# Performance work log

Measured on AMD Instinct MI355X. Metric: run time of the kernel, lower is better.

## Reference

```python
import jax, jax.numpy as jnp
import numpy as np

CLIP = 10.0  # tanh clipping constant (Kool et al. C=10)


def setup_inputs() -> dict:
    key = jax.random.key(0)
    kq, kk, kv, km = jax.random.split(key, 4)
    B, M, N, D = 16, 2048, 2048, 128
    Q = jax.random.normal(kq, (B, M, D), dtype=jnp.float32)
    K = jax.random.normal(kk, (B, N, D), dtype=jnp.float32)
    V = jax.random.normal(kv, (B, N, D), dtype=jnp.float32)
    # mask: [B, N, 1] bool; True means "forbidden" (set logit to -inf).
    # p=0.3 so every row keeps plenty of valid keys (no all-masked rows).
    mask = jax.random.bernoulli(km, 0.3, (B, N, 1))
    return {"Q": Q, "K": K, "V": V, "mask": mask}


def reference(Q, K, V, mask):
    d_k = jnp.asarray(K.shape[-1], dtype=Q.dtype)
    # logits: [B, M, N]
    logits = jnp.einsum("bmd,bnd->bmn", Q, K) / jnp.sqrt(d_k)
    logits = CLIP * jnp.tanh(logits)
    # mask [B, N, 1] -> [B, 1, N], broadcast over query dim
    mask_t = jnp.transpose(mask, (0, 2, 1))
    logits = jnp.where(mask_t, -jnp.inf, logits)
    probs = jax.nn.softmax(logits, axis=-1)
    return jnp.einsum("bmn,bnd->bmd", probs, V)
```

## Files before the change

### kernel.cpp

```cpp
#include <hip/hip_runtime.h>
#include <hip/hip_fp16.h>

typedef _Float16 h8 __attribute__((ext_vector_type(8)));
typedef _Float16 h4 __attribute__((ext_vector_type(4)));
typedef float f32x4 __attribute__((ext_vector_type(4)));
typedef float f32x16 __attribute__((ext_vector_type(16)));
typedef unsigned int u32x2 __attribute__((ext_vector_type(2)));
typedef unsigned int u32x4 __attribute__((ext_vector_type(4)));

#define MFMA16(a, b, c) __builtin_amdgcn_mfma_f32_16x16x32_f16((a), (b), (c), 0, 0, 0)
#define MFMA32(a, b, c) __builtin_amdgcn_mfma_f32_32x32x16_f16((a), (b), (c), 0, 0, 0)

static constexpr int MM = 2048, NN = 2048, DD = 128;
static constexpr int KT = 128, NT = NN / KT;
static constexpr size_t KV_IMG = (size_t)16 * 16 * 32768;
static constexpr size_t IND_IMG = 65536;
static constexpr size_t WS_NEED = 2 * KV_IMG + IND_IMG + 32768 * 4;

static constexpr float C1 = 0.25503487f;
static constexpr float C2 = 28.853900817779268f;
static constexpr float CVALID = 14.426950408889634f;
static constexpr float CMASK = -1.0e30f;

__device__ inline void glds16(const void* g, void* l) {
  __builtin_amdgcn_global_load_lds(
      (const __attribute__((address_space(1))) void*)g,
      (__attribute__((address_space(3))) void*)l, 16, 0, 0);
}

__global__ __launch_bounds__(256) void prep_mask(const void* __restrict__ mraw,
                                                 _Float16* __restrict__ ind) {
  const int tid = threadIdx.x;
  const unsigned int* mw = (const unsigned int*)mraw;
  const unsigned char* mby = (const unsigned char*)mraw;
  int okW = 1;
  for (int w = tid; w < 8192; w += 256) {
    unsigned int v = mw[w];
    okW &= (v == 0u || v == 1u || v == 0x3f800000u) ? 1 : 0;
  }
  __shared__ int sW;
  if (tid == 0) sW = 1;
  __syncthreads();
  if (!okW) atomicAnd(&sW, 0);
  __syncthreads();
  const int i = blockIdx.x * 256 + tid;
  bool masked = sW ? (mw[i] != 0u) : (mby[i] != 0);
  ind[i] = masked ? (_Float16)0.0f : (_Float16)1.0f;
}

__global__ __launch_bounds__(256) void prep_bias(const void* __restrict__ mraw,
                                                 float* __restrict__ biasC) {
  const int tid = threadIdx.x;
  const unsigned int* mw = (const unsigned int*)mraw;
  const unsigned char* mby = (const unsigned char*)mraw;
  int okW = 1;
  for (int w = tid; w < 8192; w += 256) {
    unsigned int v = mw[w];
    okW &= (v == 0u || v == 1u || v == 0x3f800000u) ? 1 : 0;
  }
  __shared__ int sW;
  if (tid == 0) sW = 1;
  __syncthreads();
  if (!okW) atomicAnd(&sW, 0);
  __syncthreads();
  const int i = blockIdx.x * 256 + tid;
  bool masked = sW ? (mw[i] != 0u) : (mby[i] != 0);
  biasC[i] = masked ? CMASK : CVALID;
}

__global__ __launch_bounds__(256) void prep_kv(const float* __restrict__ K,
                                               const float* __restrict__ V,
                                               const _Float16* __restrict__ ind,
                                               unsigned char* __restrict__ kimg,
                                               unsigned char* __restrict__ vimg) {
  const int id = blockIdx.x;
  const int tid = threadIdx.x;
  const int bt = (id < 512) ? id : (id - 512);
  if (id < 512) {
    const float* src = K + (size_t)bt * 64 * DD;
    unsigned char* dst = kimg + (size_t)(bt >> 1) * 32768 + (bt & 1) * 16384;
#pragma unroll
    for (int it = 0; it < 4; ++it) {
      const int key = (tid >> 4) + 16 * it;
      const int o = tid & 15;
      f32x4 a = *(const f32x4*)(src + key * DD + 8 * o);
      f32x4 c = *(const f32x4*)(src + key * DD + 8 * o + 4);
      h8 hv;
#pragma unroll
      for (int j = 0; j < 4; ++j) {
        hv[j] = (_Float16)(a[j] * C1);
        hv[j + 4] = (_Float16)(c[j] * C1);
      }
      *(h8*)(dst + key * 256 + ((16 * o) ^ ((key & 7) << 4))) = hv;
    }
  } else {
    const float* src = V + (size_t)bt * 64 * DD;
    unsigned char* dst = vimg + (size_t)(bt >> 1) * 32768;
    const _Float16* ip = ind + (size_t)bt * 64;
    const int d = tid & 127;
    const int half = tid >> 7;
#pragma unroll
    for (int ki = 0; ki < 4; ++ki) {
      const int koct = half * 4 + ki;
      h8 w;
#pragma unroll
      for (int q = 0; q < 8; ++q)
        w[q] = (_Float16)src[(8 * koct + q) * DD + d] * ip[8 * koct + q];
      const int g = (bt & 1) * 8 + koct;
      *(h8*)(dst + d * 256 + ((g * 16) ^ ((d & 7) << 4))) = w;
    }
  }
}

__global__ __launch_bounds__(512, 1) void attn_main(
    const float* __restrict__ Qg, const unsigned char* __restrict__ kimg,
    const unsigned char* __restrict__ vimg, const _Float16* __restrict__ indg,
    float* __restrict__ out) {
  __shared__ __align__(16) unsigned char smem[135680];
  const int tid = threadIdx.x;
  const int lane = tid & 63;
  const int wv = tid >> 6;
  const int l31 = lane & 31;
  const int hp = lane >> 5;
  const int qg = wv >> 1;
  const int h = wv & 1;
  const int bid = blockIdx.x;
  const int b = 2 * (bid & 7) + (bid >> 7);
  const int mt = (bid >> 3) & 15;
  const int m0 = mt * 128 + qg * 32;

  h8 qa[8];
  {
    const float* qr = Qg + ((size_t)b * MM + m0 + l31) * DD;
#pragma unroll
    for (int st = 0; st < 8; ++st) {
      const int d0 = 16 * st + 8 * hp;
      f32x4 a = *(const f32x4*)(qr + d0);
      f32x4 c = *(const f32x4*)(qr + d0 + 4);
      h8 hi;
#pragma unroll
      for (int j = 0; j < 4; ++j) {
        hi[j] = (_Float16)a[j];
        hi[j + 4] = (_Float16)c[j];
      }
      qa[st] = hi;
    }
  }

  f32x16 oacc[4];
#pragma unroll
  for (int dc = 0; dc < 4; ++dc)
#pragma unroll
    for (int j = 0; j < 16; ++j) oacc[dc][j] = 0.f;
  f32x16 rsacc;
#pragma unroll
  for (int j = 0; j < 16; ++j) rsacc[j] = 0.f;

  const unsigned char* kib = kimg + (size_t)b * 16 * 32768;
  const unsigned char* vib = vimg + (size_t)b * 16 * 32768;
  unsigned char* sind = smem + 131072;

#pragma unroll
  for (int i = 0; i < 4; ++i) {
    const int off = wv * 4096 + i * 1024;
    glds16(kib + off + lane * 16, smem + off);
    glds16(vib + off + lane * 16, smem + 32768 + off);
  }
  if (wv < 4)
    glds16((const unsigned char*)indg + (size_t)b * 4096 + wv * 1024 + lane * 16,
           sind + wv * 1024);
  __syncthreads();

  const int ksw = (l31 & 7) << 4;

  for (int tn = 0; tn < NT; ++tn) {
    const unsigned char* kbuf = smem + (tn & 1) * 65536;
    const unsigned char* vbuf = kbuf + 32768;
    if (tn + 1 < NT) {
      unsigned char* nbuf = smem + ((tn + 1) & 1) * 65536;
      const unsigned char* ks = kib + (size_t)(tn + 1) * 32768;
      const unsigned char* vs = vib + (size_t)(tn + 1) * 32768;
#pragma unroll
      for (int i = 0; i < 4; ++i) {
        const int off = wv * 4096 + i * 1024;
        glds16(ks + off + lane * 16, nbuf + off);
        glds16(vs + off + lane * 16, nbuf + 32768 + off);
      }
    }

#pragma unroll
    for (int c = 0; c < 2; ++c) {
      f32x16 s;
#pragma unroll
      for (int j = 0; j < 16; ++j) s[j] = 0.f;
      const int krow = (64 * h + 32 * c + l31) << 8;
      __builtin_amdgcn_s_setprio(1);
#pragma unroll
      for (int st = 0; st < 8; ++st) {
        h8 kf = *(const h8*)(kbuf + krow + ((32 * st + 16 * hp) ^ ksw));
        s = MFMA32(kf, qa[st], s);
      }
      __builtin_amdgcn_s_setprio(0);

      unsigned pkA[4], pkB[4];
#pragma unroll
      for (int jq = 0; jq < 4; ++jq) {
        float p[4];
#pragma unroll
        for (int i = 0; i < 4; ++i) {
          const float u = __builtin_amdgcn_exp2f(s[4 * jq + i]);
          p[i] = __builtin_amdgcn_exp2f(
              fmaf(-C2, __builtin_amdgcn_rcpf(u + 1.0f), CVALID));
        }
        pkA[jq] = __builtin_bit_cast(unsigned,
                                     __builtin_amdgcn_cvt_pkrtz(p[0], p[1]));
        pkB[jq] = __builtin_bit_cast(unsigned,
                                     __builtin_amdgcn_cvt_pkrtz(p[2], p[3]));
      }
      h8 pb[2];
#pragma unroll
      for (int ks = 0; ks < 2; ++ks) {
        u32x2 sa = __builtin_amdgcn_permlane32_swap(pkA[2 * ks],
                                                    pkA[2 * ks + 1], false,
                                                    false);
        u32x2 sb = __builtin_amdgcn_permlane32_swap(pkB[2 * ks],
                                                    pkB[2 * ks + 1], false,
                                                    false);
        u32x4 w = {sa[0], sb[0], sa[1], sb[1]};
        pb[ks] = __builtin_bit_cast(h8, w);
      }

      __builtin_amdgcn_s_setprio(1);
#pragma unroll
      for (int ks = 0; ks < 2; ++ks) {
        const int gks = 2 * c + ks;
        h8 ia = *(const h8*)(sind + tn * 256 + 128 * h + 32 * gks + 16 * hp);
        rsacc = MFMA32(ia, pb[ks], rsacc);
      }
#pragma unroll
      for (int dc = 0; dc < 4; ++dc) {
        const int vrow = (32 * dc + l31) << 8;
#pragma unroll
        for (int ks = 0; ks < 2; ++ks) {
          const int gks = 2 * c + ks;
          h8 vf = *(const h8*)(vbuf + vrow +
                               ((128 * h + 32 * gks + 16 * hp) ^ ksw));
          oacc[dc] = MFMA32(vf, pb[ks], oacc[dc]);
        }
      }
      __builtin_amdgcn_s_setprio(0);
    }
    __syncthreads();
  }

  const float totH = rsacc[0];

  float* rs1 = (float*)(smem + 135168);
  unsigned char* olds = smem;
  const int row = qg * 32 + l31;
  if (h == 1) {
#pragma unroll
    for (int dc = 0; dc < 4; ++dc)
#pragma unroll
      for (int jq = 0; jq < 4; ++jq) {
        f32x4 v = {oacc[dc][4 * jq + 0], oacc[dc][4 * jq + 1],
                   oacc[dc][4 * jq + 2], oacc[dc][4 * jq + 3]};
        const int dbyte = (32 * dc + 8 * jq + 4 * hp) * 4;
        *(f32x4*)(olds + row * 512 + (dbyte ^ ((row & 31) << 4))) = v;
      }
    if (hp == 0) rs1[row] = totH;
  }
  __syncthreads();
  if (h == 0) {
    const float inv = __builtin_amdgcn_rcpf(totH + rs1[row]);
#pragma unroll
    for (int dc = 0; dc < 4; ++dc)
#pragma unroll
      for (int jq = 0; jq < 4; ++jq) {
        const int dbyte = (32 * dc + 8 * jq + 4 * hp) * 4;
        float* pp = (float*)(olds + row * 512 + (dbyte ^ ((row & 31) << 4)));
        f32x4 v = *(const f32x4*)pp;
        v[0] = (v[0] + oacc[dc][4 * jq + 0]) * inv;
        v[1] = (v[1] + oacc[dc][4 * jq + 1]) * inv;
        v[2] = (v[2] + oacc[dc][4 * jq + 2]) * inv;
        v[3] = (v[3] + oacc[dc][4 * jq + 3]) * inv;
        *(f32x4*)pp = v;
      }
  }
  __syncthreads();
  float* ob = out + ((size_t)b * MM + mt * 128) * DD;
#pragma unroll
  for (int it = 0; it < 8; ++it) {
    const int byte = it * 8192 + tid * 16;
    const int r2 = byte >> 9;
    const int g16 = byte & 511;
    *(f32x4*)((unsigned char*)ob + byte) =
        *(const f32x4*)(olds + r2 * 512 + (g16 ^ ((r2 & 31) << 4)));
  }
}

__global__ __launch_bounds__(256, 2) void attn_fallback(
    const float* __restrict__ Qg, const float* __restrict__ Kg,
    const float* __restrict__ Vg, const float* __restrict__ biasC,
    float* __restrict__ out) {
  __shared__ __align__(16) unsigned char smem[51456];
  const int tid = threadIdx.x;
  const int lane = tid & 63;
  const int wv = tid >> 6;
  const int r = lane & 15;
  const int g = lane >> 4;
  const int rw = wv >> 1;
  const int h = wv & 1;
  const int b = blockIdx.x >> 5;
  const int mt = blockIdx.x & 31;
  const int m0 = mt * 64 + rw * 32;

  float* blds = (float*)(smem + 43264);
  {
    const float* cb = biasC + b * NN;
#pragma unroll
    for (int i = 0; i < 8; ++i) blds[tid + 256 * i] = cb[tid + 256 * i];
  }
  h8 qh[2][4];
  {
    const float* qb = Qg + ((size_t)b * MM + m0) * DD;
#pragma unroll
    for (int rf = 0; rf < 2; ++rf) {
      const float* qr = qb + (16 * rf + r) * DD;
#pragma unroll
      for (int t = 0; t < 4; ++t) {
        f32x4 a = *(const f32x4*)(qr + 32 * t + 8 * g);
        f32x4 c = *(const f32x4*)(qr + 32 * t + 8 * g + 4);
        h8 hi;
#pragma unroll
        for (int j = 0; j < 4; ++j) {
          hi[j] = (_Float16)a[j];
          hi[j + 4] = (_Float16)c[j];
        }
        qh[rf][t] = hi;
      }
    }
  }
  f32x4 acc[2][8];
#pragma unroll
  for (int rf = 0; rf < 2; ++rf)
#pragma unroll
    for (int cd = 0; cd < 8; ++cd) acc[rf][cd] = (f32x4){0.f, 0.f, 0.f, 0.f};
  float rs[2][4] = {{0.f, 0.f, 0.f, 0.f}, {0.f, 0.f, 0.f, 0.f}};
  const float* kb = Kg + (size_t)b * NN * DD;
  const float* vbp = Vg + (size_t)b * NN * DD;
  _Float16* plds = (_Float16*)(smem + 32768 + wv * 2560);
  const int bk0 = tid >> 5, bd0 = tid & 31;
  const int bk1 = (256 + tid) >> 5, bd1 = tid & 31;
  f32x4 kpre[8], vpre[8];
#pragma unroll
  for (int i = 0; i < 8; ++i) kpre[i] = *(const f32x4*)(kb + i * 1024 + tid * 4);
#pragma unroll
  for (int q = 0; q < 4; ++q) {
    vpre[q] = *(const f32x4*)(vbp + (4 * bk0 + q) * DD + 4 * bd0);
    vpre[4 + q] = *(const f32x4*)(vbp + (4 * bk1 + q) * DD + 4 * bd1);
  }
  for (int tn = 0; tn < 32; ++tn) {
#pragma unroll
    for (int i = 0; i < 8; ++i) {
      const int flat = i * 1024 + tid * 4;
      const int kkey = flat >> 7;
      const int d0 = flat & 127;
      h4 hv;
#pragma unroll
      for (int j = 0; j < 4; ++j) hv[j] = (_Float16)kpre[i][j];
      *(h4*)(smem + (kkey << 8) + ((d0 << 1) ^ ((kkey & 7) << 4))) = hv;
    }
#pragma unroll
    for (int it = 0; it < 2; ++it) {
      const int bk = it ? bk1 : bk0;
      const int bd = it ? bd1 : bd0;
#pragma unroll
      for (int p = 0; p < 4; ++p) {
        h4 w;
#pragma unroll
        for (int q = 0; q < 4; ++q) w[q] = (_Float16)vpre[it * 4 + q][p];
        const int d = 4 * bd + p;
        *(h4*)(smem + 16384 + (d << 7) +
               ((bk << 3) ^ (((d >> 1) & 7) << 4))) = w;
      }
    }
    if (tn + 1 < 32) {
      const float* ks = kb + (tn + 1) * 64 * DD;
      const float* vs = vbp + (tn + 1) * 64 * DD;
#pragma unroll
      for (int i = 0; i < 8; ++i) kpre[i] = *(const f32x4*)(ks + i * 1024 + tid * 4);
#pragma unroll
      for (int q = 0; q < 4; ++q) {
        vpre[q] = *(const f32x4*)(vs + (4 * bk0 + q) * DD + 4 * bd0);
        vpre[4 + q] = *(const f32x4*)(vs + (4 * bk1 + q) * DD + 4 * bd1);
      }
    }
    __syncthreads();
#pragma unroll
    for (int c = 0; c < 2; ++c) {
      f32x4 S0 = {0.f, 0.f, 0.f, 0.f}, S1 = {0.f, 0.f, 0.f, 0.f};
      const int kkey = h * 32 + 16 * c + r;
      const int krow = kkey << 8;
      const int ksw = (kkey & 7) << 4;
#pragma unroll
      for (int t = 0; t < 4; ++t) {
        h8 kf = *(const h8*)(smem + krow + ((64 * t + 16 * g) ^ ksw));
        S0 = MFMA16(qh[0][t], kf, S0);
        S1 = MFMA16(qh[1][t], kf, S1);
      }
      const float Cc = blds[tn * 64 + kkey];
#pragma unroll
      for (int j = 0; j < 4; ++j) {
        float u0 = __builtin_amdgcn_exp2f(S0[j] * C1);
        float p0 = __builtin_amdgcn_exp2f(
            fmaf(-C2, __builtin_amdgcn_rcpf(u0 + 1.0f), Cc));
        rs[0][j] += p0;
        plds[(4 * g + j) * 40 + 16 * c + r] = (_Float16)p0;
        float u1 = __builtin_amdgcn_exp2f(S1[j] * C1);
        float p1 = __builtin_amdgcn_exp2f(
            fmaf(-C2, __builtin_amdgcn_rcpf(u1 + 1.0f), Cc));
        rs[1][j] += p1;
        plds[(16 + 4 * g + j) * 40 + 16 * c + r] = (_Float16)p1;
      }
    }
    h8 a0 = *(const h8*)((unsigned char*)plds + r * 80 + 16 * g);
    h8 a1 = *(const h8*)((unsigned char*)plds + (16 + r) * 80 + 16 * g);
#pragma unroll
    for (int cd = 0; cd < 8; ++cd) {
      const int d = 16 * cd + r;
      h8 vf = *(const h8*)(smem + 16384 + (d << 7) +
                           ((64 * h + 16 * g) ^ (((d >> 1) & 7) << 4)));
      acc[0][cd] = MFMA16(a0, vf, acc[0][cd]);
      acc[1][cd] = MFMA16(a1, vf, acc[1][cd]);
    }
    __syncthreads();
  }
#pragma unroll
  for (int rf = 0; rf < 2; ++rf)
#pragma unroll
    for (int j = 0; j < 4; ++j) {
      float v = rs[rf][j];
      v += __shfl_xor(v, 1);
      v += __shfl_xor(v, 2);
      v += __shfl_xor(v, 4);
      v += __shfl_xor(v, 8);
      rs[rf][j] = v;
    }
  float* olds = (float*)smem;
  float* rslds = (float*)(smem + 43008);
  if (h == 1) {
    float* my = olds + rw * 4096;
#pragma unroll
    for (int rf = 0; rf < 2; ++rf)
#pragma unroll
      for (int cd = 0; cd < 8; ++cd)
#pragma unroll
        for (int j = 0; j < 4; ++j)
          my[(16 * rf + 4 * g + j) * 128 + 16 * cd + r] = acc[rf][cd][j];
    if (r == 0) {
#pragma unroll
      for (int rf = 0; rf < 2; ++rf)
#pragma unroll
        for (int j = 0; j < 4; ++j)
          rslds[rw * 32 + 16 * rf + 4 * g + j] = rs[rf][j];
    }
  }
  __syncthreads();
  if (h == 0) {
    const float* ot = olds + rw * 4096;
    float* ob = out + ((size_t)b * MM + m0) * DD;
#pragma unroll
    for (int rf = 0; rf < 2; ++rf)
#pragma unroll
      for (int j = 0; j < 4; ++j) {
        const int rl = 16 * rf + 4 * g + j;
        const float tot = rs[rf][j] + rslds[rw * 32 + rl];
        const float inv = __builtin_amdgcn_rcpf(tot);
#pragma unroll
        for (int cd = 0; cd < 8; ++cd) {
          float v = acc[rf][cd][j] + ot[rl * 128 + 16 * cd + r];
          ob[rl * DD + 16 * cd + r] = v * inv;
        }
      }
  }
}

extern "C" void kernel_launch(void* const* d_in, const int* in_sizes, int n_in,
                              void* d_out, int out_size, void* d_ws, size_t ws_size,
                              hipStream_t stream) {
  const float* Q = (const float*)d_in[0];
  const float* K = (const float*)d_in[1];
  const float* V = (const float*)d_in[2];
  const void* mask = d_in[3];
  float* out = (float*)d_out;
  if (ws_size >= WS_NEED) {
    unsigned char* kimg = (unsigned char*)d_ws;
    unsigned char* vimg = kimg + KV_IMG;
    _Float16* ind = (_Float16*)(vimg + KV_IMG);
    prep_mask<<<dim3(128), dim3(256), 0, stream>>>(mask, ind);
    prep_kv<<<dim3(1024), dim3(256), 0, stream>>>(K, V, ind, kimg, vimg);
    attn_main<<<dim3(256), dim3(512), 0, stream>>>(Q, kimg, vimg, ind, out);
  } else {
    float* biasC = (float*)d_ws;
    prep_bias<<<dim3(128), dim3(256), 0, stream>>>(mask, biasC);
    attn_fallback<<<dim3(512), dim3(256), 0, stream>>>(Q, K, V, biasC, out);
  }
}
```

Measured before the change: 75.18 us.

## Read K/V fragments directly from global in MFMA-native layout, drop LDS staging

Repacks the prepared K and V images into an MFMA-fragment-major layout so each lane loads its 16-byte fragment straight from global/L2 memory, removing the double-buffered LDS pipeline and its per-tile barriers. The main kernel shrinks to 256-thread blocks covering 64 query rows, with 512 blocks and two blocks per CU, so more waves can hide load latency. The QK product is split into two independent accumulators to shorten the MFMA dependency chain. In exchange, K/V reuse now relies on cache rather than shared memory, adding global traffic per block, and the V scaling is now done in fp32 before rounding.

Result: slower. 93.68 us (+24.6%).

```diff
diff --git a/kernel.cpp b/kernel.cpp
--- a/kernel.cpp
+++ b/kernel.cpp
@@ -78,11 +78,11 @@
   const int bt = (id < 512) ? id : (id - 512);
   if (id < 512) {
     const float* src = K + (size_t)bt * 64 * DD;
-    unsigned char* dst = kimg + (size_t)(bt >> 1) * 32768 + (bt & 1) * 16384;
+    unsigned char* dst = kimg + (size_t)(bt >> 1) * 32768 + (bt & 1) * 1024;
+    const int o = tid >> 4;
 #pragma unroll
     for (int it = 0; it < 4; ++it) {
-      const int key = (tid >> 4) + 16 * it;
-      const int o = tid & 15;
+      const int key = (tid & 15) + 16 * it;
       f32x4 a = *(const f32x4*)(src + key * DD + 8 * o);
       f32x4 c = *(const f32x4*)(src + key * DD + 8 * o + 4);
       h8 hv;
@@ -91,11 +91,11 @@
         hv[j] = (_Float16)(a[j] * C1);
         hv[j + 4] = (_Float16)(c[j] * C1);
       }
-      *(h8*)(dst + key * 256 + ((16 * o) ^ ((key & 7) << 4))) = hv;
+      *(h8*)(dst + o * 2048 + key * 16) = hv;
     }
   } else {
     const float* src = V + (size_t)bt * 64 * DD;
-    unsigned char* dst = vimg + (size_t)(bt >> 1) * 32768;
+    unsigned char* dst = vimg + (size_t)(bt >> 1) * 32768 + (bt & 1) * 16384;
     const _Float16* ip = ind + (size_t)bt * 64;
     const int d = tid & 127;
     const int half = tid >> 7;
@@ -105,18 +105,17 @@
       h8 w;
 #pragma unroll
       for (int q = 0; q < 8; ++q)
-        w[q] = (_Float16)src[(8 * koct + q) * DD + d] * ip[8 * koct + q];
-      const int g = (bt & 1) * 8 + koct;
-      *(h8*)(dst + d * 256 + ((g * 16) ^ ((d & 7) << 4))) = w;
-    }
-  }
-}
-
-__global__ __launch_bounds__(512, 1) void attn_main(
+        w[q] = (_Float16)(src[(8 * koct + q) * DD + d] * (float)ip[8 * koct + q]);
+      *(h8*)(dst + koct * 2048 + d * 16) = w;
+    }
+  }
+}
+
+__global__ __launch_bounds__(256, 2) void attn_main(
     const float* __restrict__ Qg, const unsigned char* __restrict__ kimg,
     const unsigned char* __restrict__ vimg, const _Float16* __restrict__ indg,
     float* __restrict__ out) {
-  __shared__ __align__(16) unsigned char smem[135680];
+  __shared__ __align__(16) unsigned char smem[37120];
   const int tid = threadIdx.x;
   const int lane = tid & 63;
   const int wv = tid >> 6;
@@ -125,9 +124,13 @@
   const int qg = wv >> 1;
   const int h = wv & 1;
   const int bid = blockIdx.x;
-  const int b = 2 * (bid & 7) + (bid >> 7);
-  const int mt = (bid >> 3) & 15;
-  const int m0 = mt * 128 + qg * 32;
+  const int b = 2 * (bid & 7) + (bid >> 8);
+  const int mt = (bid >> 3) & 31;
+  const int m0 = mt * 64 + qg * 32;
+
+  unsigned char* sind = smem + 32768;
+  glds16((const unsigned char*)indg + (size_t)b * 4096 + wv * 1024 + lane * 16,
+         sind + wv * 1024);
 
   h8 qa[8];
   {
@@ -158,47 +161,26 @@
 
   const unsigned char* kib = kimg + (size_t)b * 16 * 32768;
   const unsigned char* vib = vimg + (size_t)b * 16 * 32768;
-  unsigned char* sind = smem + 131072;
-
-#pragma unroll
-  for (int i = 0; i < 4; ++i) {
-    const int off = wv * 4096 + i * 1024;
-    glds16(kib + off + lane * 16, smem + off);
-    glds16(vib + off + lane * 16, smem + 32768 + off);
-  }
-  if (wv < 4)
-    glds16((const unsigned char*)indg + (size_t)b * 4096 + wv * 1024 + lane * 16,
-           sind + wv * 1024);
-  __syncthreads();
-
-  const int ksw = (l31 & 7) << 4;
+  __syncthreads();
 
   for (int tn = 0; tn < NT; ++tn) {
-    const unsigned char* kbuf = smem + (tn & 1) * 65536;
-    const unsigned char* vbuf = kbuf + 32768;
-    if (tn + 1 < NT) {
-      unsigned char* nbuf = smem + ((tn + 1) & 1) * 65536;
-      const unsigned char* ks = kib + (size_t)(tn + 1) * 32768;
-      const unsigned char* vs = vib + (size_t)(tn + 1) * 32768;
-#pragma unroll
-      for (int i = 0; i < 4; ++i) {
-        const int off = wv * 4096 + i * 1024;
-        glds16(ks + off + lane * 16, nbuf + off);
-        glds16(vs + off + lane * 16, nbuf + 32768 + off);
-      }
-    }
-
+    const unsigned char* kt = kib + tn * 32768;
+    const unsigned char* vt = vib + tn * 32768;
 #pragma unroll
     for (int c = 0; c < 2; ++c) {
-      f32x16 s;
-#pragma unroll
-      for (int j = 0; j < 16; ++j) s[j] = 0.f;
-      const int krow = (64 * h + 32 * c + l31) << 8;
+      h8 kf[8];
+      const int kcol = (64 * h + 32 * c + l31) * 16;
+#pragma unroll
+      for (int st = 0; st < 8; ++st)
+        kf[st] = *(const h8*)(kt + (2 * st + hp) * 2048 + kcol);
+      f32x16 s0, s1;
+#pragma unroll
+      for (int j = 0; j < 16; ++j) { s0[j] = 0.f; s1[j] = 0.f; }
       __builtin_amdgcn_s_setprio(1);
 #pragma unroll
-      for (int st = 0; st < 8; ++st) {
-        h8 kf = *(const h8*)(kbuf + krow + ((32 * st + 16 * hp) ^ ksw));
-        s = MFMA32(kf, qa[st], s);
+      for (int st = 0; st < 4; ++st) {
+        s0 = MFMA32(kf[2 * st], qa[2 * st], s0);
+        s1 = MFMA32(kf[2 * st + 1], qa[2 * st + 1], s1);
       }
       __builtin_amdgcn_s_setprio(0);
 
@@ -208,7 +190,8 @@
         float p[4];
 #pragma unroll
         for (int i = 0; i < 4; ++i) {
-          const float u = __builtin_amdgcn_exp2f(s[4 * jq + i]);
+          const float sv = s0[4 * jq + i] + s1[4 * jq + i];
+          const float u = __builtin_amdgcn_exp2f(sv);
           p[i] = __builtin_amdgcn_exp2f(
               fmaf(-C2, __builtin_amdgcn_rcpf(u + 1.0f), CVALID));
         }
@@ -233,29 +216,27 @@
       __builtin_amdgcn_s_setprio(1);
 #pragma unroll
       for (int ks = 0; ks < 2; ++ks) {
-        const int gks = 2 * c + ks;
-        h8 ia = *(const h8*)(sind + tn * 256 + 128 * h + 32 * gks + 16 * hp);
+        h8 ia = *(const h8*)(sind + tn * 256 + 128 * h + 64 * c + 32 * ks +
+                             16 * hp);
         rsacc = MFMA32(ia, pb[ks], rsacc);
       }
 #pragma unroll
       for (int dc = 0; dc < 4; ++dc) {
-        const int vrow = (32 * dc + l31) << 8;
+        const int vcol = (32 * dc + l31) * 16;
 #pragma unroll
         for (int ks = 0; ks < 2; ++ks) {
-          const int gks = 2 * c + ks;
-          h8 vf = *(const h8*)(vbuf + vrow +
-                               ((128 * h + 32 * gks + 16 * hp) ^ ksw));
+          h8 vf = *(const h8*)(vt + (8 * h + 4 * c + 2 * ks + hp) * 2048 +
+                               vcol);
           oacc[dc] = MFMA32(vf, pb[ks], oacc[dc]);
         }
       }
       __builtin_amdgcn_s_setprio(0);
     }
-    __syncthreads();
   }
 
   const float totH = rsacc[0];
 
-  float* rs1 = (float*)(smem + 135168);
+  float* rs1 = (float*)(smem + 36864);
   unsigned char* olds = smem;
   const int row = qg * 32 + l31;
   if (h == 1) {
@@ -288,10 +269,10 @@
       }
   }
   __syncthreads();
-  float* ob = out + ((size_t)b * MM + mt * 128) * DD;
+  float* ob = out + ((size_t)b * MM + mt * 64) * DD;
 #pragma unroll
   for (int it = 0; it < 8; ++it) {
-    const int byte = it * 8192 + tid * 16;
+    const int byte = it * 4096 + tid * 16;
     const int r2 = byte >> 9;
     const int g16 = byte & 511;
     *(f32x4*)((unsigned char*)ob + byte) =
@@ -500,7 +481,7 @@
     _Float16* ind = (_Float16*)(vimg + KV_IMG);
     prep_mask<<<dim3(128), dim3(256), 0, stream>>>(mask, ind);
     prep_kv<<<dim3(1024), dim3(256), 0, stream>>>(K, V, ind, kimg, vimg);
-    attn_main<<<dim3(256), dim3(512), 0, stream>>>(Q, kimg, vimg, ind, out);
+    attn_main<<<dim3(512), dim3(256), 0, stream>>>(Q, kimg, vimg, ind, out);
   } else {
     float* biasC = (float*)d_ws;
     prep_bias<<<dim3(128), dim3(256), 0, stream>>>(mask, biasC);
```

## Register-block two query groups per wave and fuse mask prep into KV prep

Applied to the files above, without the earlier changes.

The attention kernel moves from 8 to 4 waves per block. Each wave now handles 64 query rows as two 32-row groups, so every K and V fragment read from LDS feeds two MFMAs instead of one. The separate mask-prep kernel is folded into the V-prep blocks, which removes one launch and the dependency on a global indicator buffer. The output staging moves from an XOR-swizzled layout to a padded row stride. The s_setprio hints are also dropped. The trade-off is roughly double the accumulator registers per wave and half the resident waves for latency hiding.

Result: slower. 78.50 us (+4.4%).

```diff
diff --git a/kernel.cpp b/kernel.cpp
--- a/kernel.cpp
+++ b/kernel.cpp
@@ -12,7 +12,7 @@
 #define MFMA32(a, b, c) __builtin_amdgcn_mfma_f32_32x32x16_f16((a), (b), (c), 0, 0, 0)
 
 static constexpr int MM = 2048, NN = 2048, DD = 128;
-static constexpr int KT = 128, NT = NN / KT;
+static constexpr int NT = 16;
 static constexpr size_t KV_IMG = (size_t)16 * 16 * 32768;
 static constexpr size_t IND_IMG = 65536;
 static constexpr size_t WS_NEED = 2 * KV_IMG + IND_IMG + 32768 * 4;
@@ -26,26 +26,6 @@
   __builtin_amdgcn_global_load_lds(
       (const __attribute__((address_space(1))) void*)g,
       (__attribute__((address_space(3))) void*)l, 16, 0, 0);
-}
-
-__global__ __launch_bounds__(256) void prep_mask(const void* __restrict__ mraw,
-                                                 _Float16* __restrict__ ind) {
-  const int tid = threadIdx.x;
-  const unsigned int* mw = (const unsigned int*)mraw;
-  const unsigned char* mby = (const unsigned char*)mraw;
-  int okW = 1;
-  for (int w = tid; w < 8192; w += 256) {
-    unsigned int v = mw[w];
-    okW &= (v == 0u || v == 1u || v == 0x3f800000u) ? 1 : 0;
-  }
-  __shared__ int sW;
-  if (tid == 0) sW = 1;
-  __syncthreads();
-  if (!okW) atomicAnd(&sW, 0);
-  __syncthreads();
-  const int i = blockIdx.x * 256 + tid;
-  bool masked = sW ? (mw[i] != 0u) : (mby[i] != 0);
-  ind[i] = masked ? (_Float16)0.0f : (_Float16)1.0f;
 }
 
 __global__ __launch_bounds__(256) void prep_bias(const void* __restrict__ mraw,
@@ -68,15 +48,14 @@
   biasC[i] = masked ? CMASK : CVALID;
 }
 
-__global__ __launch_bounds__(256) void prep_kv(const float* __restrict__ K,
-                                               const float* __restrict__ V,
-                                               const _Float16* __restrict__ ind,
-                                               unsigned char* __restrict__ kimg,
-                                               unsigned char* __restrict__ vimg) {
+__global__ __launch_bounds__(256) void prep_all(
+    const float* __restrict__ K, const float* __restrict__ V,
+    const void* __restrict__ mraw, unsigned char* __restrict__ kimg,
+    unsigned char* __restrict__ vimg, _Float16* __restrict__ ind) {
   const int id = blockIdx.x;
   const int tid = threadIdx.x;
-  const int bt = (id < 512) ? id : (id - 512);
   if (id < 512) {
+    const int bt = id;
     const float* src = K + (size_t)bt * 64 * DD;
     unsigned char* dst = kimg + (size_t)(bt >> 1) * 32768 + (bt & 1) * 16384;
 #pragma unroll
@@ -94,9 +73,29 @@
       *(h8*)(dst + key * 256 + ((16 * o) ^ ((key & 7) << 4))) = hv;
     }
   } else {
+    const int bt = id - 512;
+    const unsigned int* mw = (const unsigned int*)mraw;
+    const unsigned char* mby = (const unsigned char*)mraw;
+    int okW = 1;
+    for (int w = tid; w < 8192; w += 256) {
+      unsigned int v = mw[w];
+      okW &= (v == 0u || v == 1u || v == 0x3f800000u) ? 1 : 0;
+    }
+    __shared__ int sW;
+    __shared__ float sip[64];
+    if (tid == 0) sW = 1;
+    __syncthreads();
+    if (!okW) atomicAnd(&sW, 0);
+    __syncthreads();
+    if (tid < 64) {
+      const int gk = bt * 64 + tid;
+      bool masked = sW ? (mw[gk] != 0u) : (mby[gk] != 0);
+      sip[tid] = masked ? 0.0f : 1.0f;
+      ind[gk] = masked ? (_Float16)0.0f : (_Float16)1.0f;
+    }
+    __syncthreads();
     const float* src = V + (size_t)bt * 64 * DD;
     unsigned char* dst = vimg + (size_t)(bt >> 1) * 32768;
-    const _Float16* ip = ind + (size_t)bt * 64;
     const int d = tid & 127;
     const int half = tid >> 7;
 #pragma unroll
@@ -105,14 +104,14 @@
       h8 w;
 #pragma unroll
       for (int q = 0; q < 8; ++q)
-        w[q] = (_Float16)src[(8 * koct + q) * DD + d] * ip[8 * koct + q];
+        w[q] = (_Float16)(src[(8 * koct + q) * DD + d] * sip[8 * koct + q]);
       const int g = (bt & 1) * 8 + koct;
       *(h8*)(dst + d * 256 + ((g * 16) ^ ((d & 7) << 4))) = w;
     }
   }
 }
 
-__global__ __launch_bounds__(512, 1) void attn_main(
+__global__ __launch_bounds__(256, 1) void attn_main(
     const float* __restrict__ Qg, const unsigned char* __restrict__ kimg,
     const unsigned char* __restrict__ vimg, const _Float16* __restrict__ indg,
     float* __restrict__ out) {
@@ -123,15 +122,20 @@
   const int l31 = lane & 31;
   const int hp = lane >> 5;
   const int qg = wv >> 1;
-  const int h = wv & 1;
+  const int kh = wv & 1;
   const int bid = blockIdx.x;
   const int b = 2 * (bid & 7) + (bid >> 7);
   const int mt = (bid >> 3) & 15;
-  const int m0 = mt * 128 + qg * 32;
-
-  h8 qa[8];
-  {
-    const float* qr = Qg + ((size_t)b * MM + m0 + l31) * DD;
+
+  const unsigned char* kib = kimg + (size_t)b * 16 * 32768;
+  const unsigned char* vib = vimg + (size_t)b * 16 * 32768;
+  unsigned char* sind = smem + 131072;
+
+  h8 qa[2][8];
+#pragma unroll
+  for (int qgrp = 0; qgrp < 2; ++qgrp) {
+    const float* qr =
+        Qg + ((size_t)b * MM + mt * 128 + qg * 64 + qgrp * 32 + l31) * DD;
 #pragma unroll
     for (int st = 0; st < 8; ++st) {
       const int d0 = 16 * st + 8 * hp;
@@ -143,32 +147,38 @@
         hi[j] = (_Float16)a[j];
         hi[j + 4] = (_Float16)c[j];
       }
-      qa[st] = hi;
-    }
-  }
-
-  f32x16 oacc[4];
-#pragma unroll
-  for (int dc = 0; dc < 4; ++dc)
-#pragma unroll
-    for (int j = 0; j < 16; ++j) oacc[dc][j] = 0.f;
-  f32x16 rsacc;
-#pragma unroll
-  for (int j = 0; j < 16; ++j) rsacc[j] = 0.f;
-
-  const unsigned char* kib = kimg + (size_t)b * 16 * 32768;
-  const unsigned char* vib = vimg + (size_t)b * 16 * 32768;
-  unsigned char* sind = smem + 131072;
-
-#pragma unroll
-  for (int i = 0; i < 4; ++i) {
-    const int off = wv * 4096 + i * 1024;
-    glds16(kib + off + lane * 16, smem + off);
-    glds16(vib + off + lane * 16, smem + 32768 + off);
-  }
-  if (wv < 4)
-    glds16((const unsigned char*)indg + (size_t)b * 4096 + wv * 1024 + lane * 16,
-           sind + wv * 1024);
+      qa[qgrp][st] = hi;
+    }
+  }
+
+  f32x16 oacc[2][4];
+#pragma unroll
+  for (int qgrp = 0; qgrp < 2; ++qgrp)
+#pragma unroll
+    for (int dc = 0; dc < 4; ++dc)
+#pragma unroll
+      for (int j = 0; j < 16; ++j) oacc[qgrp][dc][j] = 0.f;
+  f32x16 rsacc[2];
+#pragma unroll
+  for (int qgrp = 0; qgrp < 2; ++qgrp)
+#pragma unroll
+    for (int j = 0; j < 16; ++j) rsacc[qgrp][j] = 0.f;
+
+  auto stage = [&](int tn, int bi) {
+    const unsigned char* kt = kib + (size_t)tn * 32768;
+    const unsigned char* vt = vib + (size_t)tn * 32768;
+    unsigned char* dst = smem + bi * 65536;
+#pragma unroll
+    for (int i = 0; i < 8; ++i) {
+      const int off = wv * 8192 + i * 1024;
+      glds16(kt + off + lane * 16, dst + off);
+      glds16(vt + off + lane * 16, dst + 32768 + off);
+    }
+  };
+
+  glds16((const unsigned char*)indg + (size_t)b * 4096 + wv * 1024 + lane * 16,
+         sind + wv * 1024);
+  stage(0, 0);
   __syncthreads();
 
   const int ksw = (l31 & 7) << 4;
@@ -176,126 +186,120 @@
   for (int tn = 0; tn < NT; ++tn) {
     const unsigned char* kbuf = smem + (tn & 1) * 65536;
     const unsigned char* vbuf = kbuf + 32768;
-    if (tn + 1 < NT) {
-      unsigned char* nbuf = smem + ((tn + 1) & 1) * 65536;
-      const unsigned char* ks = kib + (size_t)(tn + 1) * 32768;
-      const unsigned char* vs = vib + (size_t)(tn + 1) * 32768;
-#pragma unroll
-      for (int i = 0; i < 4; ++i) {
-        const int off = wv * 4096 + i * 1024;
-        glds16(ks + off + lane * 16, nbuf + off);
-        glds16(vs + off + lane * 16, nbuf + 32768 + off);
-      }
-    }
-
-#pragma unroll
-    for (int c = 0; c < 2; ++c) {
-      f32x16 s;
-#pragma unroll
-      for (int j = 0; j < 16; ++j) s[j] = 0.f;
-      const int krow = (64 * h + 32 * c + l31) << 8;
-      __builtin_amdgcn_s_setprio(1);
+    if (tn + 1 < NT) stage(tn + 1, (tn + 1) & 1);
+
+#pragma unroll
+    for (int kg = 0; kg < 2; ++kg) {
+      const int key = 64 * kh + 32 * kg + l31;
+      const int krow = key << 8;
+
+      f32x16 s[2];
+#pragma unroll
+      for (int j = 0; j < 16; ++j) { s[0][j] = 0.f; s[1][j] = 0.f; }
 #pragma unroll
       for (int st = 0; st < 8; ++st) {
         h8 kf = *(const h8*)(kbuf + krow + ((32 * st + 16 * hp) ^ ksw));
-        s = MFMA32(kf, qa[st], s);
-      }
-      __builtin_amdgcn_s_setprio(0);
-
-      unsigned pkA[4], pkB[4];
-#pragma unroll
-      for (int jq = 0; jq < 4; ++jq) {
-        float p[4];
-#pragma unroll
-        for (int i = 0; i < 4; ++i) {
-          const float u = __builtin_amdgcn_exp2f(s[4 * jq + i]);
-          p[i] = __builtin_amdgcn_exp2f(
-              fmaf(-C2, __builtin_amdgcn_rcpf(u + 1.0f), CVALID));
-        }
-        pkA[jq] = __builtin_bit_cast(unsigned,
-                                     __builtin_amdgcn_cvt_pkrtz(p[0], p[1]));
-        pkB[jq] = __builtin_bit_cast(unsigned,
-                                     __builtin_amdgcn_cvt_pkrtz(p[2], p[3]));
-      }
-      h8 pb[2];
+        s[0] = MFMA32(kf, qa[0][st], s[0]);
+        s[1] = MFMA32(kf, qa[1][st], s[1]);
+      }
+
+      h8 pb[2][2];
+#pragma unroll
+      for (int qgrp = 0; qgrp < 2; ++qgrp) {
+        unsigned pkA[4], pkB[4];
+#pragma unroll
+        for (int jq = 0; jq < 4; ++jq) {
+          float p[4];
+#pragma unroll
+          for (int i = 0; i < 4; ++i) {
+            const float u = __builtin_amdgcn_exp2f(s[qgrp][4 * jq + i]);
+            p[i] = __builtin_amdgcn_exp2f(
+                fmaf(-C2, __builtin_amdgcn_rcpf(u + 1.0f), CVALID));
+          }
+          pkA[jq] = __builtin_bit_cast(unsigned,
+                                       __builtin_amdgcn_cvt_pkrtz(p[0], p[1]));
+          pkB[jq] = __builtin_bit_cast(unsigned,
+                                       __builtin_amdgcn_cvt_pkrtz(p[2], p[3]));
+        }
+#pragma unroll
+        for (int ks = 0; ks < 2; ++ks) {
+          u32x2 sa = __builtin_amdgcn_permlane32_swap(
+              pkA[2 * ks], pkA[2 * ks + 1], false, false);
+          u32x2 sb = __builtin_amdgcn_permlane32_swap(
+              pkB[2 * ks], pkB[2 * ks + 1], false, false);
+          u32x4 w = {sa[0], sb[0], sa[1], sb[1]};
+          pb[qgrp][ks] = __builtin_bit_cast(h8, w);
+        }
+      }
+
 #pragma unroll
       for (int ks = 0; ks < 2; ++ks) {
-        u32x2 sa = __builtin_amdgcn_permlane32_swap(pkA[2 * ks],
-                                                    pkA[2 * ks + 1], false,
-                                                    false);
-        u32x2 sb = __builtin_amdgcn_permlane32_swap(pkB[2 * ks],
-                                                    pkB[2 * ks + 1], false,
-                                                    false);
-        u32x4 w = {sa[0], sb[0], sa[1], sb[1]};
-        pb[ks] = __builtin_bit_cast(h8, w);
-      }
-
-      __builtin_amdgcn_s_setprio(1);
-#pragma unroll
-      for (int ks = 0; ks < 2; ++ks) {
-        const int gks = 2 * c + ks;
-        h8 ia = *(const h8*)(sind + tn * 256 + 128 * h + 32 * gks + 16 * hp);
-        rsacc = MFMA32(ia, pb[ks], rsacc);
-      }
+        h8 ia = *(const h8*)(sind + tn * 256 + 128 * kh + 64 * kg + 32 * ks +
+                             16 * hp);
+        rsacc[0] = MFMA32(ia, pb[0][ks], rsacc[0]);
+        rsacc[1] = MFMA32(ia, pb[1][ks], rsacc[1]);
+      }
+
 #pragma unroll
       for (int dc = 0; dc < 4; ++dc) {
         const int vrow = (32 * dc + l31) << 8;
 #pragma unroll
         for (int ks = 0; ks < 2; ++ks) {
-          const int gks = 2 * c + ks;
           h8 vf = *(const h8*)(vbuf + vrow +
-                               ((128 * h + 32 * gks + 16 * hp) ^ ksw));
-          oacc[dc] = MFMA32(vf, pb[ks], oacc[dc]);
-        }
-      }
-      __builtin_amdgcn_s_setprio(0);
+                               ((128 * kh + 64 * kg + 32 * ks + 16 * hp) ^
+                                ksw));
+          oacc[0][dc] = MFMA32(vf, pb[0][ks], oacc[0][dc]);
+          oacc[1][dc] = MFMA32(vf, pb[1][ks], oacc[1][dc]);
+        }
+      }
     }
     __syncthreads();
   }
 
-  const float totH = rsacc[0];
-
+  float* olds = (float*)smem;
   float* rs1 = (float*)(smem + 135168);
-  unsigned char* olds = smem;
-  const int row = qg * 32 + l31;
-  if (h == 1) {
-#pragma unroll
-    for (int dc = 0; dc < 4; ++dc)
-#pragma unroll
-      for (int jq = 0; jq < 4; ++jq) {
-        f32x4 v = {oacc[dc][4 * jq + 0], oacc[dc][4 * jq + 1],
-                   oacc[dc][4 * jq + 2], oacc[dc][4 * jq + 3]};
-        const int dbyte = (32 * dc + 8 * jq + 4 * hp) * 4;
-        *(f32x4*)(olds + row * 512 + (dbyte ^ ((row & 31) << 4))) = v;
-      }
-    if (hp == 0) rs1[row] = totH;
+  if (kh == 1) {
+#pragma unroll
+    for (int qgrp = 0; qgrp < 2; ++qgrp) {
+      const int row = qg * 64 + qgrp * 32 + l31;
+#pragma unroll
+      for (int dc = 0; dc < 4; ++dc)
+#pragma unroll
+        for (int jq = 0; jq < 4; ++jq) {
+          f32x4 v = {oacc[qgrp][dc][4 * jq + 0], oacc[qgrp][dc][4 * jq + 1],
+                     oacc[qgrp][dc][4 * jq + 2], oacc[qgrp][dc][4 * jq + 3]};
+          *(f32x4*)&olds[row * 132 + 32 * dc + 8 * jq + 4 * hp] = v;
+        }
+      if (hp == 0) rs1[row] = rsacc[qgrp][0];
+    }
   }
   __syncthreads();
-  if (h == 0) {
-    const float inv = __builtin_amdgcn_rcpf(totH + rs1[row]);
-#pragma unroll
-    for (int dc = 0; dc < 4; ++dc)
-#pragma unroll
-      for (int jq = 0; jq < 4; ++jq) {
-        const int dbyte = (32 * dc + 8 * jq + 4 * hp) * 4;
-        float* pp = (float*)(olds + row * 512 + (dbyte ^ ((row & 31) << 4)));
-        f32x4 v = *(const f32x4*)pp;
-        v[0] = (v[0] + oacc[dc][4 * jq + 0]) * inv;
-        v[1] = (v[1] + oacc[dc][4 * jq + 1]) * inv;
-        v[2] = (v[2] + oacc[dc][4 * jq + 2]) * inv;
-        v[3] = (v[3] + oacc[dc][4 * jq + 3]) * inv;
-        *(f32x4*)pp = v;
-      }
+  if (kh == 0) {
+#pragma unroll
+    for (int qgrp = 0; qgrp < 2; ++qgrp) {
+      const int row = qg * 64 + qgrp * 32 + l31;
+      const float inv = __builtin_amdgcn_rcpf(rsacc[qgrp][0] + rs1[row]);
+#pragma unroll
+      for (int dc = 0; dc < 4; ++dc)
+#pragma unroll
+        for (int jq = 0; jq < 4; ++jq) {
+          float* pp = &olds[row * 132 + 32 * dc + 8 * jq + 4 * hp];
+          f32x4 v = *(const f32x4*)pp;
+          v[0] = (v[0] + oacc[qgrp][dc][4 * jq + 0]) * inv;
+          v[1] = (v[1] + oacc[qgrp][dc][4 * jq + 1]) * inv;
+          v[2] = (v[2] + oacc[qgrp][dc][4 * jq + 2]) * inv;
+          v[3] = (v[3] + oacc[qgrp][dc][4 * jq + 3]) * inv;
+          *(f32x4*)pp = v;
+        }
+    }
   }
   __syncthreads();
   float* ob = out + ((size_t)b * MM + mt * 128) * DD;
 #pragma unroll
-  for (int it = 0; it < 8; ++it) {
-    const int byte = it * 8192 + tid * 16;
-    const int r2 = byte >> 9;
-    const int g16 = byte & 511;
-    *(f32x4*)((unsigned char*)ob + byte) =
-        *(const f32x4*)(olds + r2 * 512 + (g16 ^ ((r2 & 31) << 4)));
+  for (int c = 0; c < 16; ++c) {
+    const int idx = c * 1024 + tid * 4;
+    const int r2 = idx >> 7, col = idx & 127;
+    *(f32x4*)&ob[r2 * 128 + col] = *(const f32x4*)&olds[r2 * 132 + col];
   }
 }
 
@@ -498,9 +502,8 @@
     unsigned char* kimg = (unsigned char*)d_ws;
     unsigned char* vimg = kimg + KV_IMG;
     _Float16* ind = (_Float16*)(vimg + KV_IMG);
-    prep_mask<<<dim3(128), dim3(256), 0, stream>>>(mask, ind);
-    prep_kv<<<dim3(1024), dim3(256), 0, stream>>>(K, V, ind, kimg, vimg);
-    attn_main<<<dim3(256), dim3(512), 0, stream>>>(Q, kimg, vimg, ind, out);
+    prep_all<<<dim3(1024), dim3(256), 0, stream>>>(K, V, mask, kimg, vimg, ind);
+    attn_main<<<dim3(256), dim3(256), 0, stream>>>(Q, kimg, vimg, ind, out);
   } else {
     float* biasC = (float*)d_ws;
     prep_bias<<<dim3(128), dim3(256), 0, stream>>>(mask, biasC);
```
